# Performance work log

Hardware: AMD Instinct MI355X
Metric: run time of the kernel (lower is better)

Reference implementation:

```python
import jax, jax.numpy as jnp
import numpy as np

K = 16                 # hardcoded k in KL_divergence default
TYPICAL_CRLB = 0.15 * 100 / 10   # = 1.5, sigma used in KL divergence


def setup_inputs() -> dict:
    key = jax.random.key(0)
    k1, k2 = jax.random.split(key)
    N = 8192
    ch1 = jax.random.normal(k1, (N, 2), dtype=jnp.float32)
    ch2 = jax.random.normal(k2, (N, 2), dtype=jnp.float32)
    # Polynomial layer parameters, exactly as in __init__ (identity-ish map)
    M1 = jnp.array([[0.0, 0.0], [1.0, 0.0]], dtype=jnp.float32)
    M2 = jnp.array([[0.0, 1.0], [0.0, 0.0]], dtype=jnp.float32)
    return {"ch1": ch1, "ch2": ch2, "M1": M1, "M2": M2}


def _polynomial(x, M1, M2):
    # out[:,0] = sum_ij M1[i,j] * x1^i * x2^j ; out[:,1] analog with M2 (m=2)
    x1, x2 = x[:, 0], x[:, 1]
    pi = jnp.stack([jnp.ones_like(x1), x1], axis=1)          # [N,2] -> x1^i
    pj = jnp.stack([jnp.ones_like(x2), x2], axis=1)          # [N,2] -> x2^j
    B = pi[:, :, None] * pj[:, None, :]                      # [N,2,2] basis x1^i*x2^j
    y1 = jnp.einsum('nij,ij->n', B, M1)
    y2 = jnp.einsum('nij,ij->n', B, M2)
    return jnp.stack([y1, y2], axis=1)                       # [N,2]


def reference(ch1, ch2, M1, M2):
    N = ch1.shape[0]
    ch2m = _polynomial(ch2, M1, M2)

    # --- KNN ---
    diff = ch1[None, :, :] - ch2m[:, None, :]                # [N2, N1, 2]
    distances = diff * diff                                  # squared per-coord dists
    abs_distances = jnp.sum(distances, axis=2)               # [N2, N1]
    # top_k of negated transposed distances: for each ch1 point, k nearest ch2m
    _, idx = jax.lax.top_k(-abs_distances.T, K)              # [N1, K] indices into ch2 axis
    # Faithful reproduction of the original index construction:
    # idx is flattened row-major ([N,K]); indx1 flattens a [K,N] arange-broadcast,
    # so the second coordinate at flat position t is t % N.
    flat_a = idx.reshape(-1)                                 # [N*K] indexes axis 0 (ch2)
    flat_b = jnp.tile(jnp.arange(N), K)                      # [N*K] indexes axis 1 (ch1)
    knn = distances[flat_a, flat_b].reshape(K, N, 2)         # [K, N, 2]

    # --- KL divergence ---
    sigma2 = TYPICAL_CRLB
    D_KL = 0.5 * jnp.sum(knn / (sigma2 ** 2), axis=2)        # [K, N]

    # --- Rel entropy ---
    expD = jnp.sum(jnp.exp(-D_KL), axis=0) / N               # [N]
    mask = expD != 0.0                                       # tf boolean_mask of nonzeros
    safe = jnp.where(mask, expD, 1.0)
    return -jnp.sum(jnp.where(mask, jnp.log(safe), 0.0))
```

## Files before the change

kernel.cpp:

```cpp
#include <hip/hip_runtime.h>
#include <math.h>
#include <stdint.h>

#define K_NN 16
#define NPTS 8192
#define NR 32

static __device__ __constant__ float d_bt[33] = {
    -3.4028235e38f,
    -1.8627318f, -1.5341205f, -1.3180109f, -1.1503494f, -1.0100762f,
    -0.8871466f, -0.7764218f, -0.6744898f, -0.5791322f, -0.4887764f,
    -0.4022501f, -0.3186394f, -0.2372021f, -0.1573107f, -0.0784124f,
     0.0f,
     0.0784124f,  0.1573107f,  0.2372021f,  0.3186394f,  0.4022501f,
     0.4887764f,  0.5791322f,  0.6744898f,  0.7764218f,  0.8871466f,
     1.0100762f,  1.1503494f,  1.3180109f,  1.5341205f,  1.8627318f,
     3.4028235e38f
};

__device__ __forceinline__ int rowOf(const float* bt, float y) {
    int c = 0;
    c += (y >= bt[c + 16]) ? 16 : 0;
    c += (y >= bt[c + 8])  ? 8  : 0;
    c += (y >= bt[c + 4])  ? 4  : 0;
    c += (y >= bt[c + 2])  ? 2  : 0;
    c += (y >= bt[c + 1])  ? 1  : 0;
    return c;
}

__global__ __launch_bounds__(1024) void kb_build(const float* __restrict__ ch2,
                                                 const float* __restrict__ M1,
                                                 const float* __restrict__ M2,
                                                 float2* __restrict__ spts,
                                                 int* __restrict__ sidx,
                                                 int* __restrict__ rowStart,
                                                 float* __restrict__ out) {
    __shared__ int h[NR];
    __shared__ int offs[NR];
    __shared__ float bt[33];
    const int tid = threadIdx.x;
    if (tid == 0) out[0] = 0.0f;
    if (tid < 33) bt[tid] = d_bt[tid];
    if (tid < NR) h[tid] = 0;
    __syncthreads();

    const float a0 = M1[0], a1 = M1[1], a2 = M1[2], a3 = M1[3];
    const float b0 = M2[0], b1 = M2[1], b2 = M2[2], b3 = M2[3];

    for (int i = tid; i < NPTS; i += 1024) {
        float2 v = ((const float2*)ch2)[i];
        float py = b0 + b1 * v.y + v.x * (b2 + b3 * v.y);
        atomicAdd(&h[rowOf(bt, py)], 1);
    }
    __syncthreads();

    if (tid == 0) {
        int run = 0;
        for (int r = 0; r < NR; ++r) { offs[r] = run; rowStart[r] = run; run += h[r]; }
        rowStart[NR] = run;
    }
    __syncthreads();

    for (int i = tid; i < NPTS; i += 1024) {
        float2 v = ((const float2*)ch2)[i];
        float px = a0 + a1 * v.y + v.x * (a2 + a3 * v.y);
        float py = b0 + b1 * v.y + v.x * (b2 + b3 * v.y);
        int pos = atomicAdd(&offs[rowOf(bt, py)], 1);
        spts[pos] = make_float2(px, py);
        sidx[pos] = i;
    }
}

__global__ __launch_bounds__(1024) void kq_query(const float* __restrict__ ch1,
                                                 const float2* __restrict__ spts,
                                                 const int* __restrict__ gsidx,
                                                 const int* __restrict__ rowStart,
                                                 int* __restrict__ midx) {
    __shared__ float2 shp[NPTS];

    const int tid  = threadIdx.x;
    const int lane = tid & 63;
    const int w    = tid >> 6;
    const int qg   = blockIdx.x * 16 + w;

#pragma unroll
    for (int e = 0; e < 4; ++e)
        ((float4*)shp)[e * 1024 + tid] = ((const float4*)spts)[e * 1024 + tid];

    int btb = __float_as_int(d_bt[lane < 33 ? lane : 0]);
    int rsv = rowStart[lane < 33 ? lane : 0];
    __syncthreads();

    const float qx = ch1[2 * qg + 0];
    const float qy = ch1[2 * qg + 1];

    int own = rowOf(d_bt, qy);

    unsigned key = 0xFFFFFFFFu;
    unsigned thr = 0xFFFFFFFFu;
    bool first = true;

#define SCAN_ROW(R)                                                            \
    {                                                                          \
        int lo = __builtin_amdgcn_readlane(rsv, (R));                          \
        int hi = __builtin_amdgcn_readlane(rsv, (R) + 1);                      \
        for (int base = lo; base < hi; base += 64) {                           \
            int i = base + lane;                                               \
            bool act = i < hi;                                                 \
            int ii = act ? i : (hi - 1);                                       \
            float2 p = shp[ii];                                                \
            int si = gsidx[ii];                                                \
            float dx = qx - p.x, dy = qy - p.y;                                \
            unsigned u = act ? __float_as_uint(dx * dx + dy * dy)              \
                             : 0xFFFFFFFFu;                                    \
            if (first) {                                                       \
                first = false;                                                 \
                unsigned mn = min(u, (unsigned)__shfl_xor((int)u, 1, 64));     \
                mn = min(mn, (unsigned)__shfl_xor((int)mn, 2, 64));            \
                unsigned mx = mn;                                              \
                mx = max(mx, (unsigned)__shfl_xor((int)mx, 4, 64));            \
                mx = max(mx, (unsigned)__shfl_xor((int)mx, 8, 64));            \
                mx = max(mx, (unsigned)__shfl_xor((int)mx, 16, 64));           \
                mx = max(mx, (unsigned)__shfl_xor((int)mx, 32, 64));           \
                thr = mx | 0x1FFFu;                                            \
            }                                                                  \
            unsigned nk = (u & 0xFFFFE000u) | (unsigned)si;                    \
            unsigned long long m = __ballot(u <= thr);                         \
            while (m) {                                                        \
                int l = __ffsll(m) - 1;                                        \
                m &= m - 1;                                                    \
                unsigned snk = (unsigned)__builtin_amdgcn_readlane((int)nk, l);\
                unsigned up = (unsigned)__builtin_amdgcn_update_dpp(           \
                    0, (int)key, 0x111, 0xF, 0xF, false);       \
                bool c1 = snk < key;                                           \
                unsigned nv = (snk < up) ? up : snk;                           \
                key = c1 ? nv : key;                                           \
            }                                                                  \
            thr = (unsigned)__builtin_amdgcn_readlane((int)key, 15) | 0x1FFFu; \
        }                                                                      \
    }

    SCAN_ROW(own)

    bool loDone = false, hiDone = false;
    for (int d = 1; d < NR; ++d) {
        unsigned kthT = thr & 0xFFFFE000u;
        int rlo = own - d, rhi = own + d;
        if (!loDone) {
            if (rlo < 0) loDone = true;
            else {
                float band = qy - __uint_as_float(
                    __builtin_amdgcn_readlane(btb, rlo + 1));
                unsigned bb = __float_as_uint(band * band) & 0xFFFFE000u;
                if (bb > kthT) loDone = true;
                else SCAN_ROW(rlo)
            }
        }
        if (!hiDone) {
            if (rhi > NR - 1) hiDone = true;
            else {
                float band = __uint_as_float(
                    __builtin_amdgcn_readlane(btb, rhi)) - qy;
                unsigned bb = __float_as_uint(band * band) & 0xFFFFE000u;
                if (bb > (thr & 0xFFFFE000u)) hiDone = true;
                else SCAN_ROW(rhi)
            }
        }
        if (loDone && hiDone) break;
    }
#undef SCAN_ROW

    if (lane < K_NN)
        midx[qg * K_NN + lane] = (int)(key & 0x1FFFu);
}

__global__ __launch_bounds__(1024) void k3_final(const float* __restrict__ ch1,
                                                 const float* __restrict__ ch2,
                                                 const float* __restrict__ M1,
                                                 const float* __restrict__ M2,
                                                 const int* __restrict__ midx,
                                                 float* __restrict__ out, int N) {
    const float a0 = M1[0], a1 = M1[1], a2 = M1[2], a3 = M1[3];
    const float b0 = M2[0], b1 = M2[1], b2 = M2[2], b3 = M2[3];

    int t = blockIdx.x * 1024 + threadIdx.x;
    int n = t >> 4;
    int k = t & 15;
    int g = n >> 4;
    int r = n & 15;

    int j = k * (N / K_NN) + g;
    int a = midx[j * K_NN + r];
    float2 cp = ((const float2*)ch2)[a];
    float cx = a0 + a1 * cp.y + cp.x * (a2 + a3 * cp.y);
    float cy = b0 + b1 * cp.y + cp.x * (b2 + b3 * cp.y);
    float dx = ch1[2 * n + 0] - cx;
    float dy = ch1[2 * n + 1] - cy;
    float term = expf(-(dx * dx + dy * dy) * (1.0f / 4.5f));

#pragma unroll
    for (int off = 8; off; off >>= 1) term += __shfl_down(term, off, 16);

    float v = 0.0f;
    if (k == 0) {
        float expD = term / (float)N;
        v = (expD != 0.0f) ? logf(expD) : 0.0f;
    }
#pragma unroll
    for (int off = 32; off; off >>= 1) v += __shfl_down(v, off, 64);

    __shared__ float red[16];
    int lane = threadIdx.x & 63;
    int wv = threadIdx.x >> 6;
    if (lane == 0) red[wv] = v;
    __syncthreads();
    if (threadIdx.x == 0) {
        float s = 0.0f;
#pragma unroll
        for (int i = 0; i < 16; ++i) s += red[i];
        atomicAdd(out, -s);
    }
}

extern "C" void kernel_launch(void* const* d_in, const int* in_sizes, int n_in,
                              void* d_out, int out_size, void* d_ws, size_t ws_size,
                              hipStream_t stream) {
    const float* ch1 = (const float*)d_in[0];
    const float* ch2 = (const float*)d_in[1];
    const float* M1  = (const float*)d_in[2];
    const float* M2  = (const float*)d_in[3];
    float* out = (float*)d_out;
    const int N = in_sizes[0] / 2;

    char* ws = (char*)d_ws;
    float2* spts     = (float2*)ws;
    int*    sidx     = (int*)(ws + 65536);
    int*    rowStart = (int*)(ws + 65536 + 32768);
    int*    midx     = (int*)(ws + 65536 + 32768 + 256);

    kb_build<<<1, 1024, 0, stream>>>(ch2, M1, M2, spts, sidx, rowStart, out);

    kq_query<<<N / 16, 1024, 0, stream>>>(ch1, spts, sidx, rowStart, midx);

    k3_final<<<(N * K_NN) / 1024, 1024, 0, stream>>>(ch1, ch2, M1, M2, midx, out, N);
}
```

Baseline: 100.8 us.

## Pack point indices into float mantissa bits and scan two points per lane

Removes the separate global sorted-index array by packing each point's 13-bit original index into the low mantissa bits of its x and y coordinates. The build kernel now bins points in shared memory with rows padded to even length, so the query kernel can read two points per lane with a float4 LDS load. Each pass covers 128 candidates instead of 64 and no longer does a global gsidx load per candidate. Truncating mantissa bits slightly perturbs the distances, and the second ballot loop adds serial insertion work.

```diff
diff --git a/kernel.cpp b/kernel.cpp
--- a/kernel.cpp
+++ b/kernel.cpp
@@ -5,6 +5,7 @@
 #define K_NN 16
 #define NPTS 8192
 #define NR 32
+#define PADN (NPTS + 64)
 
 static __device__ __constant__ float d_bt[33] = {
     -3.4028235e38f,
@@ -32,9 +33,9 @@
                                                  const float* __restrict__ M1,
                                                  const float* __restrict__ M2,
                                                  float2* __restrict__ spts,
-                                                 int* __restrict__ sidx,
                                                  int* __restrict__ rowStart,
                                                  float* __restrict__ out) {
+    __shared__ float2 lsp[PADN];
     __shared__ int h[NR];
     __shared__ int offs[NR];
     __shared__ float bt[33];
@@ -42,59 +43,76 @@
     if (tid == 0) out[0] = 0.0f;
     if (tid < 33) bt[tid] = d_bt[tid];
     if (tid < NR) h[tid] = 0;
+    const float inf = __int_as_float(0x7F800000);
+    for (int i = tid; i < PADN; i += 1024) lsp[i] = make_float2(inf, inf);
     __syncthreads();
 
     const float a0 = M1[0], a1 = M1[1], a2 = M1[2], a3 = M1[3];
     const float b0 = M2[0], b1 = M2[1], b2 = M2[2], b3 = M2[3];
-
-    for (int i = tid; i < NPTS; i += 1024) {
-        float2 v = ((const float2*)ch2)[i];
-        float py = b0 + b1 * v.y + v.x * (b2 + b3 * v.y);
-        atomicAdd(&h[rowOf(bt, py)], 1);
+    const float4* __restrict__ g4 = (const float4*)ch2;
+
+    float2 pts[8];
+    int rw[8];
+#pragma unroll
+    for (int e = 0; e < 4; ++e) {
+        float4 v = g4[e * 1024 + tid];
+        pts[2 * e]     = make_float2(a0 + a1 * v.y + v.x * (a2 + a3 * v.y),
+                                     b0 + b1 * v.y + v.x * (b2 + b3 * v.y));
+        pts[2 * e + 1] = make_float2(a0 + a1 * v.w + v.z * (a2 + a3 * v.w),
+                                     b0 + b1 * v.w + v.z * (b2 + b3 * v.w));
+    }
+#pragma unroll
+    for (int p = 0; p < 8; ++p) {
+        rw[p] = rowOf(bt, pts[p].y);
+        atomicAdd(&h[rw[p]], 1);
     }
     __syncthreads();
 
     if (tid == 0) {
         int run = 0;
-        for (int r = 0; r < NR; ++r) { offs[r] = run; rowStart[r] = run; run += h[r]; }
+        for (int r = 0; r < NR; ++r) {
+            offs[r] = run;
+            rowStart[r] = run;
+            run += (h[r] + 1) & ~1;
+        }
         rowStart[NR] = run;
     }
     __syncthreads();
 
-    for (int i = tid; i < NPTS; i += 1024) {
-        float2 v = ((const float2*)ch2)[i];
-        float px = a0 + a1 * v.y + v.x * (a2 + a3 * v.y);
-        float py = b0 + b1 * v.y + v.x * (b2 + b3 * v.y);
-        int pos = atomicAdd(&offs[rowOf(bt, py)], 1);
-        spts[pos] = make_float2(px, py);
-        sidx[pos] = i;
-    }
+#pragma unroll
+    for (int p = 0; p < 8; ++p) {
+        int gi = 2 * ((p >> 1) * 1024 + tid) + (p & 1);
+        int pos = atomicAdd(&offs[rw[p]], 1);
+        unsigned ux = (__float_as_uint(pts[p].x) & ~0x7Fu) | ((unsigned)gi >> 6);
+        unsigned uy = (__float_as_uint(pts[p].y) & ~0x3Fu) | ((unsigned)gi & 63u);
+        lsp[pos] = make_float2(__uint_as_float(ux), __uint_as_float(uy));
+    }
+    __syncthreads();
+
+    for (int i = tid; i < PADN / 2; i += 1024)
+        ((float4*)spts)[i] = ((float4*)lsp)[i];
 }
 
 __global__ __launch_bounds__(1024) void kq_query(const float* __restrict__ ch1,
                                                  const float2* __restrict__ spts,
-                                                 const int* __restrict__ gsidx,
                                                  const int* __restrict__ rowStart,
                                                  int* __restrict__ midx) {
-    __shared__ float2 shp[NPTS];
-
+    __shared__ float2 shp[PADN];
     const int tid  = threadIdx.x;
     const int lane = tid & 63;
     const int w    = tid >> 6;
     const int qg   = blockIdx.x * 16 + w;
 
-#pragma unroll
-    for (int e = 0; e < 4; ++e)
-        ((float4*)shp)[e * 1024 + tid] = ((const float4*)spts)[e * 1024 + tid];
-
+    for (int i = tid; i < PADN / 2; i += 1024)
+        ((float4*)shp)[i] = ((const float4*)spts)[i];
+
+    int rsv = rowStart[lane < 33 ? lane : 0];
     int btb = __float_as_int(d_bt[lane < 33 ? lane : 0]);
-    int rsv = rowStart[lane < 33 ? lane : 0];
     __syncthreads();
 
     const float qx = ch1[2 * qg + 0];
     const float qy = ch1[2 * qg + 1];
-
-    int own = rowOf(d_bt, qy);
+    const int own = rowOf(d_bt, qy);
 
     unsigned key = 0xFFFFFFFFu;
     unsigned thr = 0xFFFFFFFFu;
@@ -103,19 +121,23 @@
 #define SCAN_ROW(R)                                                            \
     {                                                                          \
         int lo = __builtin_amdgcn_readlane(rsv, (R));                          \
-        int hi = __builtin_amdgcn_readlane(rsv, (R) + 1);                      \
-        for (int base = lo; base < hi; base += 64) {                           \
-            int i = base + lane;                                               \
-            bool act = i < hi;                                                 \
-            int ii = act ? i : (hi - 1);                                       \
-            float2 p = shp[ii];                                                \
-            int si = gsidx[ii];                                                \
-            float dx = qx - p.x, dy = qy - p.y;                                \
-            unsigned u = act ? __float_as_uint(dx * dx + dy * dy)              \
+        int hi = __builtin_amdgcn_readlane(rsv, (R) + 1);       \
+        for (int base = lo; base < hi; base += 128) {                          \
+            int i0 = base + 2 * lane;                                          \
+            int ii = min(i0, hi - 2);                         \
+            float4 cc = *(const float4*)&shp[ii];                              \
+            bool a0 = i0 < hi;                                                 \
+            bool a1 = i0 + 1 < hi;                                             \
+            float dx0 = qx - cc.x, dy0 = qy - cc.y;                            \
+            float dx1 = qx - cc.z, dy1 = qy - cc.w;                            \
+            unsigned u0 = a0 ? __float_as_uint(dx0 * dx0 + dy0 * dy0)          \
+                             : 0xFFFFFFFFu;                                    \
+            unsigned u1 = a1 ? __float_as_uint(dx1 * dx1 + dy1 * dy1)          \
                              : 0xFFFFFFFFu;                                    \
             if (first) {                                                       \
                 first = false;                                                 \
-                unsigned mn = min(u, (unsigned)__shfl_xor((int)u, 1, 64));     \
+                unsigned mn = min(u0, u1);                                     \
+                mn = min(mn, (unsigned)__shfl_xor((int)mn, 1, 64));            \
                 mn = min(mn, (unsigned)__shfl_xor((int)mn, 2, 64));            \
                 unsigned mx = mn;                                              \
                 mx = max(mx, (unsigned)__shfl_xor((int)mx, 4, 64));            \
@@ -124,18 +146,34 @@
                 mx = max(mx, (unsigned)__shfl_xor((int)mx, 32, 64));           \
                 thr = mx | 0x1FFFu;                                            \
             }                                                                  \
-            unsigned nk = (u & 0xFFFFE000u) | (unsigned)si;                    \
-            unsigned long long m = __ballot(u <= thr);                         \
-            while (m) {                                                        \
-                int l = __ffsll(m) - 1;                                        \
-                m &= m - 1;                                                    \
-                unsigned snk = (unsigned)__builtin_amdgcn_readlane((int)nk, l);\
+            unsigned id0 = ((__float_as_uint(cc.x) & 0x7Fu) << 6)              \
+                         | (__float_as_uint(cc.y) & 0x3Fu);                    \
+            unsigned id1 = ((__float_as_uint(cc.z) & 0x7Fu) << 6)              \
+                         | (__float_as_uint(cc.w) & 0x3Fu);                    \
+            unsigned nk0 = (u0 & 0xFFFFE000u) | id0;                           \
+            unsigned nk1 = (u1 & 0xFFFFE000u) | id1;                           \
+            unsigned long long m0 = __ballot(u0 <= thr);                       \
+            unsigned long long m1 = __ballot(u1 <= thr);                       \
+            while (m0) {                                                       \
+                int l = __ffsll(m0) - 1;                                       \
+                m0 &= m0 - 1;                                                  \
+                unsigned snk = (unsigned)__builtin_amdgcn_readlane((int)nk0, l);\
                 unsigned up = (unsigned)__builtin_amdgcn_update_dpp(           \
                     0, (int)key, 0x111, 0xF, 0xF, false);       \
                 bool c1 = snk < key;                                           \
                 unsigned nv = (snk < up) ? up : snk;                           \
                 key = c1 ? nv : key;                                           \
             }                                                                  \
+            while (m1) {                                                       \
+                int l = __ffsll(m1) - 1;                                       \
+                m1 &= m1 - 1;                                                  \
+                unsigned snk = (unsigned)__builtin_amdgcn_readlane((int)nk1, l);\
+                unsigned up = (unsigned)__builtin_amdgcn_update_dpp(           \
+                    0, (int)key, 0x111, 0xF, 0xF, false);                      \
+                bool c1 = snk < key;                                           \
+                unsigned nv = (snk < up) ? up : snk;                           \
+                key = c1 ? nv : key;                                           \
+            }                                                                  \
             thr = (unsigned)__builtin_amdgcn_readlane((int)key, 15) | 0x1FFFu; \
         }                                                                      \
     }
@@ -144,7 +182,6 @@
 
     bool loDone = false, hiDone = false;
     for (int d = 1; d < NR; ++d) {
-        unsigned kthT = thr & 0xFFFFE000u;
         int rlo = own - d, rhi = own + d;
         if (!loDone) {
             if (rlo < 0) loDone = true;
@@ -152,7 +189,7 @@
                 float band = qy - __uint_as_float(
                     __builtin_amdgcn_readlane(btb, rlo + 1));
                 unsigned bb = __float_as_uint(band * band) & 0xFFFFE000u;
-                if (bb > kthT) loDone = true;
+                if (bb > (thr & 0xFFFFE000u)) loDone = true;
                 else SCAN_ROW(rlo)
             }
         }
@@ -234,13 +271,12 @@
 
     char* ws = (char*)d_ws;
     float2* spts     = (float2*)ws;
-    int*    sidx     = (int*)(ws + 65536);
-    int*    rowStart = (int*)(ws + 65536 + 32768);
-    int*    midx     = (int*)(ws + 65536 + 32768 + 256);
-
-    kb_build<<<1, 1024, 0, stream>>>(ch2, M1, M2, spts, sidx, rowStart, out);
-
-    kq_query<<<N / 16, 1024, 0, stream>>>(ch1, spts, sidx, rowStart, midx);
+    int*    rowStart = (int*)(ws + 66560);
+    int*    midx     = (int*)(ws + 66560 + 256);
+
+    kb_build<<<1, 1024, 0, stream>>>(ch2, M1, M2, spts, rowStart, out);
+
+    kq_query<<<N / 16, 1024, 0, stream>>>(ch1, spts, rowStart, midx);
 
     k3_final<<<(N * K_NN) / 1024, 1024, 0, stream>>>(ch1, ch2, M1, M2, midx, out, N);
 }
```

Result: faster. 89.82 us (-10.9%).
